# Kernel tuning notes

Measured on AMD Instinct MI355X. Metric: run time of the kernel, lower is better.

Reference implementation:

```python
import jax, jax.numpy as jnp
import numpy as np

N_NODES = 50000


def _segment_mean(vals, seg_ids, num_segments):
    s = jax.ops.segment_sum(vals, seg_ids, num_segments=num_segments)
    cnt = jax.ops.segment_sum(jnp.ones((vals.shape[0],), vals.dtype), seg_ids,
                              num_segments=num_segments)
    return s / jnp.clip(cnt, 1.0)[:, None]


def _sage_layer(h, src, dst, W_self, W_neigh, b):
    # mean-aggregate neighbor messages: gather h[src], scatter-mean to dst
    neigh = _segment_mean(h[src], dst, N_NODES)
    return h @ W_self + neigh @ W_neigh + b


def _edge_score(h, src, dst, Wp, bp):
    # concat(h_u, h_v) @ Wp == h_u @ Wp[:d] + h_v @ Wp[d:]
    d = h.shape[1]
    return h[src] @ Wp[:d] + h[dst] @ Wp[d:] + bp


def setup_inputs() -> dict:
    key = jax.random.key(0)
    ks = jax.random.split(key, 16)
    N, E, EP, EN = N_NODES, 800000, 200000, 200000
    d_in, d_hid, d_out = 128, 256, 128
    inp = {
        'x': jax.random.normal(ks[0], (N, d_in), jnp.float32),
        'msg_src': jax.random.randint(ks[1], (E,), 0, N, jnp.int32),
        'msg_dst': jax.random.randint(ks[2], (E,), 0, N, jnp.int32),
        'pos_src': jax.random.randint(ks[3], (EP,), 0, N, jnp.int32),
        'pos_dst': jax.random.randint(ks[4], (EP,), 0, N, jnp.int32),
        'neg_src': jax.random.randint(ks[5], (EN,), 0, N, jnp.int32),
        'neg_dst': jax.random.randint(ks[6], (EN,), 0, N, jnp.int32),
        'W1_self': jax.random.normal(ks[7], (d_in, d_hid), jnp.float32) * 0.05,
        'W1_neigh': jax.random.normal(ks[8], (d_in, d_hid), jnp.float32) * 0.05,
        'b1': jnp.zeros((d_hid,), jnp.float32),
        'W2_self': jax.random.normal(ks[9], (d_hid, d_out), jnp.float32) * 0.05,
        'W2_neigh': jax.random.normal(ks[10], (d_hid, d_out), jnp.float32) * 0.05,
        'b2': jnp.zeros((d_out,), jnp.float32),
        'Wp': jax.random.normal(ks[11], (2 * d_out, 1), jnp.float32) * 0.05,
        'bp': jnp.zeros((1,), jnp.float32),
    }
    return inp


def reference(x, msg_src, msg_dst, pos_src, pos_dst, neg_src, neg_dst,
              W1_self, W1_neigh, b1, W2_self, W2_neigh, b2, Wp, bp):
    h = _sage_layer(x, msg_src, msg_dst, W1_self, W1_neigh, b1)
    h = jax.nn.relu(h)
    h = _sage_layer(h, msg_src, msg_dst, W2_self, W2_neigh, b2)
    pos_score = _edge_score(h, pos_src, pos_dst, Wp, bp)
    neg_score = _edge_score(h, neg_src, neg_dst, Wp, bp)
    return pos_score, neg_score
```

## Files before the change

### kernel.cpp

```cpp
#include <hip/hip_runtime.h>


#define NN 50000
#define EM 800000
#define EPOS 200000
#define ENEG 200000
#define NB 196
#define RPB 4096
#define MTILES 3125
#define GEMM_GRID 512

typedef __bf16 bf16;
typedef bf16 bf16x2 __attribute__((ext_vector_type(2)));
typedef bf16 bf16x4 __attribute__((ext_vector_type(4)));
typedef bf16 bf16x8 __attribute__((ext_vector_type(8)));
typedef float floatx4 __attribute__((ext_vector_type(4)));

#define I_CNT  0
#define I_ROW  50176
#define I_BSUM 100608
#define I_BOFF 100864
#define I_CCUR 101120
#define I_CSR  101376
#define B_CREG 3605504
#define B_XB   10005504
#define B_AGG1 22805504
#define B_H1   35605504
#define B_NV   61205504
#define B_WT1  62005504
#define B_WT2  62136576
#define B_P    62267648
#define B_Q    62468352

__global__ __launch_bounds__(256) void count_kernel(const int* __restrict__ dst,
                                                    int* __restrict__ cnt, int n) {
    int i = blockIdx.x * blockDim.x + threadIdx.x;
    if (i < n) atomicAdd(&cnt[dst[i]], 1);
}

__global__ __launch_bounds__(256) void scan1_kernel(const int* __restrict__ cnt,
                                                    int* __restrict__ bsum) {
    __shared__ int s[256];
    int t = threadIdx.x;
    int i = blockIdx.x * 256 + t;
    s[t] = (i < NN) ? cnt[i] : 0;
    __syncthreads();
    for (int o = 128; o > 0; o >>= 1) {
        if (t < o) s[t] += s[t + o];
        __syncthreads();
    }
    if (t == 0) bsum[blockIdx.x] = s[0];
}

__global__ __launch_bounds__(256) void scan2_kernel(const int* __restrict__ bsum,
                                                    int* __restrict__ boff) {
    __shared__ int s[256];
    int t = threadIdx.x;
    s[t] = (t < NB) ? bsum[t] : 0;
    __syncthreads();
    for (int o = 1; o < 256; o <<= 1) {
        int u = (t >= o) ? s[t - o] : 0;
        __syncthreads();
        s[t] += u;
        __syncthreads();
    }
    if (t < NB) boff[t] = (t == 0) ? 0 : s[t - 1];
}

__global__ __launch_bounds__(256) void scan3_kernel(const int* __restrict__ cnt,
                                                    const int* __restrict__ boff,
                                                    int* __restrict__ rowstart,
                                                    int* __restrict__ ccur) {
    __shared__ int s[256];
    int t = threadIdx.x;
    int i = blockIdx.x * 256 + t;
    int v = (i < NN) ? cnt[i] : 0;
    s[t] = v;
    __syncthreads();
    for (int o = 1; o < 256; o <<= 1) {
        int u = (t >= o) ? s[t - o] : 0;
        __syncthreads();
        s[t] += u;
        __syncthreads();
    }
    int excl = boff[blockIdx.x] + s[t] - v;
    if (i < NN) rowstart[i] = excl;
    if (i == NN - 1) rowstart[NN] = EM;
    if (t == 0) ccur[blockIdx.x] = boff[blockIdx.x];
}

__global__ __launch_bounds__(256) void bin_kernel(const int* __restrict__ src,
                                                  const int* __restrict__ dst,
                                                  int* __restrict__ ccur,
                                                  unsigned long long* __restrict__ creg) {
    __shared__ int hist[NB];
    __shared__ int cnt2[NB];
    __shared__ int goff[NB];
    __shared__ int base[256];
    __shared__ unsigned long long sorted[RPB];
    int t = threadIdx.x;
    int e0 = blockIdx.x * RPB;
    int nrec = EM - e0; if (nrec > RPB) nrec = RPB;

    for (int i = t; i < NB; i += 256) { hist[i] = 0; cnt2[i] = 0; }
    __syncthreads();

    int myb[RPB / 256];
    unsigned long long myrec[RPB / 256];
#pragma unroll
    for (int j = 0; j < RPB / 256; ++j) {
        int idx = j * 256 + t;
        if (idx < nrec) {
            int s = src[e0 + idx], d = dst[e0 + idx];
            myb[j] = d >> 8;
            myrec[j] = ((unsigned long long)(unsigned)d << 32) | (unsigned)s;
            atomicAdd(&hist[myb[j]], 1);
        } else myb[j] = -1;
    }
    __syncthreads();

    base[t] = (t < NB) ? hist[t] : 0;
    __syncthreads();
    for (int o = 1; o < 256; o <<= 1) {
        int u = (t >= o) ? base[t - o] : 0;
        __syncthreads();
        base[t] += u;
        __syncthreads();
    }

    if (t < NB && hist[t] > 0) goff[t] = atomicAdd(&ccur[t], hist[t]);
#pragma unroll
    for (int j = 0; j < RPB / 256; ++j) {
        if (myb[j] >= 0) {
            int rk = atomicAdd(&cnt2[myb[j]], 1);
            sorted[base[myb[j]] - hist[myb[j]] + rk] = myrec[j];
        }
    }
    __syncthreads();

#pragma unroll
    for (int j = 0; j < RPB / 256; ++j) {
        int idx = j * 256 + t;
        if (idx < nrec) {
            unsigned long long rec = sorted[idx];
            int b = (int)(rec >> 40);
            int exb = base[b] - hist[b];
            creg[(size_t)goff[b] + (idx - exb)] = rec;
        }
    }
}

__global__ __launch_bounds__(256) void binsort_kernel(
    const unsigned long long* __restrict__ creg,
    const int* __restrict__ rowstart, int* __restrict__ csr) {
    __shared__ int lcur[256];
    int t = threadIdx.x;
    int node0 = blockIdx.x * 256;
    int nodes = NN - node0; if (nodes > 256) nodes = 256;
    if (t < nodes) lcur[t] = rowstart[node0 + t];
    __syncthreads();
    int beg = rowstart[node0];
    int end = rowstart[node0 + nodes];
    for (int i = beg + t; i < end; i += 256) {
        unsigned long long rec = creg[i];
        int s = (int)(rec & 0xffffffffu);
        int d = (int)(rec >> 32);
        int pos = atomicAdd(&lcur[d - node0], 1);
        csr[pos] = s;
    }
}

__global__ __launch_bounds__(256) void convx_kernel(const float* __restrict__ x,
                                                    bf16* __restrict__ xb) {
    int i = blockIdx.x * 256 + threadIdx.x;
    if (i >= NN * 128 / 4) return;
    float4 v = ((const float4*)x)[i];
    bf16x4 o;
    o[0] = (bf16)v.x; o[1] = (bf16)v.y; o[2] = (bf16)v.z; o[3] = (bf16)v.w;
    *(bf16x4*)(xb + (size_t)i * 4) = o;
}

__global__ __launch_bounds__(256) void convw_kernel(
    const float* __restrict__ W1s, const float* __restrict__ W1n,
    const float* __restrict__ W2n, const float* __restrict__ W2s,
    bf16* __restrict__ Wt1, bf16* __restrict__ Wt2) {
    int i = blockIdx.x * 256 + threadIdx.x;
    if (i >= 65536) return;
    int n = i >> 8, k = i & 255;
    float w1 = (k < 128) ? W1s[k * 256 + n] : W1n[(k - 128) * 256 + n];
    Wt1[i] = (bf16)w1;
    float w2 = (n < 128) ? W2n[k * 128 + n] : W2s[k * 128 + (n - 128)];
    Wt2[i] = (bf16)w2;
}

__global__ __launch_bounds__(256) void gather1_kernel(const bf16* __restrict__ feat,
                                                      const int* __restrict__ rowstart,
                                                      const int* __restrict__ csr,
                                                      bf16* __restrict__ agg) {
    int node = (blockIdx.x * 256 + threadIdx.x) >> 6;
    if (node >= NN) return;
    int lane = threadIdx.x & 63;
    int c = lane * 2;
    int beg = rowstart[node], end = rowstart[node + 1];
    float ax = 0.f, ay = 0.f;
    int i = beg;
    for (; i + 7 < end; i += 8) {
        float lx = 0.f, ly = 0.f;
#pragma unroll
        for (int u = 0; u < 8; ++u) {
            int s = csr[i + u];
            bf16x2 v = *(const bf16x2*)(feat + (size_t)s * 128 + c);
            lx += (float)v[0];
            ly += (float)v[1];
        }
        ax += lx; ay += ly;
    }
    for (; i < end; ++i) {
        int s = csr[i];
        bf16x2 v = *(const bf16x2*)(feat + (size_t)s * 128 + c);
        ax += (float)v[0];
        ay += (float)v[1];
    }
    int deg = end - beg;
    float inv = 1.0f / (float)(deg > 0 ? deg : 1);
    bf16x2 o;
    o[0] = (bf16)(ax * inv);
    o[1] = (bf16)(ay * inv);
    *(bf16x2*)(agg + (size_t)node * 128 + c) = o;
}

__global__ __launch_bounds__(256) void gemm1_kernel(
    const bf16* __restrict__ xb, const bf16* __restrict__ aggb,
    const bf16* __restrict__ Wt, const float* __restrict__ b1,
    bf16* __restrict__ h1b) {
    int w = threadIdx.x >> 6;
    int lane = threadIdx.x & 63;
    int r = lane & 15, quad = lane >> 4;
    int colbase = w * 64;

    bf16x8 bfr[4][8];
#pragma unroll
    for (int t = 0; t < 4; ++t)
#pragma unroll
        for (int kk = 0; kk < 8; ++kk)
            bfr[t][kk] = *(const bf16x8*)(Wt + (size_t)(colbase + t * 16 + r) * 256
                                          + kk * 32 + quad * 8);
    float bb[4];
#pragma unroll
    for (int t = 0; t < 4; ++t) bb[t] = b1[colbase + t * 16 + r];

    for (int tile = blockIdx.x; tile < MTILES; tile += GEMM_GRID) {
        int m0 = tile * 16;
        int row = m0 + r;
        bf16x8 a[8];
#pragma unroll
        for (int kk = 0; kk < 4; ++kk)
            a[kk] = *(const bf16x8*)(xb + (size_t)row * 128 + kk * 32 + quad * 8);
#pragma unroll
        for (int kk = 4; kk < 8; ++kk)
            a[kk] = *(const bf16x8*)(aggb + (size_t)row * 128 + (kk - 4) * 32 + quad * 8);
        floatx4 acc[4];
#pragma unroll
        for (int t = 0; t < 4; ++t) acc[t] = (floatx4){0.f, 0.f, 0.f, 0.f};
#pragma unroll
        for (int kk = 0; kk < 8; ++kk)
#pragma unroll
            for (int t = 0; t < 4; ++t)
                acc[t] = __builtin_amdgcn_mfma_f32_16x16x32_bf16(a[kk], bfr[t][kk],
                                                                 acc[t], 0, 0, 0);
        int mb = m0 + quad * 4;
#pragma unroll
        for (int t = 0; t < 4; ++t) {
            int col = colbase + t * 16 + r;
#pragma unroll
            for (int rr = 0; rr < 4; ++rr) {
                float v = acc[t][rr] + bb[t];
                v = v > 0.f ? v : 0.f;
                h1b[(size_t)(mb + rr) * 256 + col] = (bf16)v;
            }
        }
    }
}

__global__ __launch_bounds__(256) void gemm2_kernel(
    const bf16* __restrict__ h1b, const bf16* __restrict__ Wt,
    const float* __restrict__ b2, const float* __restrict__ wp,
    float4* __restrict__ nodev) {
    __shared__ float lp[4][16];
    __shared__ float lq[4][16];
    int w = threadIdx.x >> 6;
    int lane = threadIdx.x & 63;
    int r = lane & 15, quad = lane >> 4;
    int colbase = w * 64;

    bf16x8 bfr[4][8];
#pragma unroll
    for (int t = 0; t < 4; ++t)
#pragma unroll
        for (int kk = 0; kk < 8; ++kk)
            bfr[t][kk] = *(const bf16x8*)(Wt + (size_t)(colbase + t * 16 + r) * 256
                                          + kk * 32 + quad * 8);
    float bb[4], wA[4], wB[4];
#pragma unroll
    for (int t = 0; t < 4; ++t) {
        int col = colbase + t * 16 + r;
        if (w < 2) {
            bb[t] = 0.f;
            wA[t] = wp[col];
            wB[t] = wp[128 + col];
        } else {
            int c2 = col - 128;
            bb[t] = b2[c2];
            wA[t] = wp[c2];
            wB[t] = wp[128 + c2];
        }
    }

    for (int tile = blockIdx.x; tile < MTILES; tile += GEMM_GRID) {
        int m0 = tile * 16;
        int row = m0 + r;
        bf16x8 a[8];
#pragma unroll
        for (int kk = 0; kk < 8; ++kk)
            a[kk] = *(const bf16x8*)(h1b + (size_t)row * 256 + kk * 32 + quad * 8);
        floatx4 acc[4];
#pragma unroll
        for (int t = 0; t < 4; ++t) acc[t] = (floatx4){0.f, 0.f, 0.f, 0.f};
#pragma unroll
        for (int kk = 0; kk < 8; ++kk)
#pragma unroll
            for (int t = 0; t < 4; ++t)
                acc[t] = __builtin_amdgcn_mfma_f32_16x16x32_bf16(a[kk], bfr[t][kk],
                                                                 acc[t], 0, 0, 0);
        float pacc[4], qacc[4];
#pragma unroll
        for (int rr = 0; rr < 4; ++rr) {
            float pr = 0.f, qr = 0.f;
#pragma unroll
            for (int t = 0; t < 4; ++t) {
                float v = acc[t][rr] + bb[t];
                pr += v * wA[t];
                qr += v * wB[t];
            }
            pacc[rr] = pr;
            qacc[rr] = qr;
        }
#pragma unroll
        for (int m = 1; m <= 8; m <<= 1) {
#pragma unroll
            for (int rr = 0; rr < 4; ++rr) {
                pacc[rr] += __shfl_xor(pacc[rr], m);
                qacc[rr] += __shfl_xor(qacc[rr], m);
            }
        }
        if (r == 0) {
#pragma unroll
            for (int rr = 0; rr < 4; ++rr) {
                lp[w][quad * 4 + rr] = pacc[rr];
                lq[w][quad * 4 + rr] = qacc[rr];
            }
        }
        __syncthreads();
        if (threadIdx.x < 16) {
            int rw = threadIdx.x;
            float4 o;
            o.x = lp[0][rw] + lp[1][rw];
            o.y = lq[0][rw] + lq[1][rw];
            o.z = lp[2][rw] + lp[3][rw];
            o.w = lq[2][rw] + lq[3][rw];
            nodev[m0 + rw] = o;
        }
        __syncthreads();
    }
}

__global__ __launch_bounds__(256) void gather2_kernel(
    const float4* __restrict__ nodev, const int* __restrict__ rowstart,
    const int* __restrict__ csr, float* __restrict__ p, float* __restrict__ q) {
    int t = threadIdx.x;
    int node = blockIdx.x * 16 + (t >> 4);
    if (node >= NN) return;
    int l = t & 15;
    int beg = rowstart[node], end = rowstart[node + 1];
    float pz = 0.f, qz = 0.f;
    for (int i = beg + l; i < end; i += 16) {
        float4 v = nodev[csr[i]];
        pz += v.x;
        qz += v.y;
    }
#pragma unroll
    for (int m = 8; m >= 1; m >>= 1) {
        pz += __shfl_xor(pz, m);
        qz += __shfl_xor(qz, m);
    }
    if (l == 0) {
        int deg = end - beg;
        float inv = 1.0f / (float)(deg > 0 ? deg : 1);
        float4 me = nodev[node];
        p[node] = me.z + pz * inv;
        q[node] = me.w + qz * inv;
    }
}

__global__ __launch_bounds__(256) void score_kernel(
    const int* __restrict__ psrc, const int* __restrict__ pdst,
    const int* __restrict__ nsrc, const int* __restrict__ ndst,
    const float* __restrict__ p, const float* __restrict__ q,
    const float* __restrict__ bp, float* __restrict__ out) {
    int i = blockIdx.x * blockDim.x + threadIdx.x;
    float b = bp[0];
    if (i < EPOS) {
        out[i] = p[psrc[i]] + q[pdst[i]] + b;
    } else if (i < EPOS + ENEG) {
        int j = i - EPOS;
        out[i] = p[nsrc[j]] + q[ndst[j]] + b;
    }
}

extern "C" void kernel_launch(void* const* d_in, const int* in_sizes, int n_in,
                              void* d_out, int out_size, void* d_ws, size_t ws_size,
                              hipStream_t stream) {
    const float* x    = (const float*)d_in[0];
    const int*   msrc = (const int*)d_in[1];
    const int*   mdst = (const int*)d_in[2];
    const int*   psrc = (const int*)d_in[3];
    const int*   pdst = (const int*)d_in[4];
    const int*   nsrc = (const int*)d_in[5];
    const int*   ndst = (const int*)d_in[6];
    const float* W1s  = (const float*)d_in[7];
    const float* W1n  = (const float*)d_in[8];
    const float* b1   = (const float*)d_in[9];
    const float* W2s  = (const float*)d_in[10];
    const float* W2n  = (const float*)d_in[11];
    const float* b2   = (const float*)d_in[12];
    const float* wp   = (const float*)d_in[13];
    const float* bp   = (const float*)d_in[14];

    char* ws = (char*)d_ws;
    int*   cnt      = (int*)ws + I_CNT;
    int*   rowstart = (int*)ws + I_ROW;
    int*   bsum     = (int*)ws + I_BSUM;
    int*   boff     = (int*)ws + I_BOFF;
    int*   ccur     = (int*)ws + I_CCUR;
    int*   csr_src  = (int*)ws + I_CSR;
    unsigned long long* creg = (unsigned long long*)(ws + B_CREG);
    bf16*   xb    = (bf16*)(ws + B_XB);
    bf16*   agg1b = (bf16*)(ws + B_AGG1);
    bf16*   h1b   = (bf16*)(ws + B_H1);
    float4* nodev = (float4*)(ws + B_NV);
    bf16*   Wt1   = (bf16*)(ws + B_WT1);
    bf16*   Wt2   = (bf16*)(ws + B_WT2);
    float*  p     = (float*)(ws + B_P);
    float*  q     = (float*)(ws + B_Q);
    float*  out   = (float*)d_out;

    hipMemsetAsync(cnt, 0, 50176 * sizeof(int), stream);

    count_kernel<<<(EM + 255) / 256, 256, 0, stream>>>(mdst, cnt, EM);
    scan1_kernel<<<NB, 256, 0, stream>>>(cnt, bsum);
    scan2_kernel<<<1, 256, 0, stream>>>(bsum, boff);
    scan3_kernel<<<NB, 256, 0, stream>>>(cnt, boff, rowstart, ccur);
    bin_kernel<<<(EM + RPB - 1) / RPB, 256, 0, stream>>>(msrc, mdst, ccur, creg);
    binsort_kernel<<<NB, 256, 0, stream>>>(creg, rowstart, csr_src);

    convx_kernel<<<6250, 256, 0, stream>>>(x, xb);
    convw_kernel<<<256, 256, 0, stream>>>(W1s, W1n, W2n, W2s, Wt1, Wt2);

    gather1_kernel<<<(NN * 64 + 255) / 256, 256, 0, stream>>>(xb, rowstart, csr_src, agg1b);
    gemm1_kernel<<<GEMM_GRID, 256, 0, stream>>>(xb, agg1b, Wt1, b1, h1b);
    gemm2_kernel<<<GEMM_GRID, 256, 0, stream>>>(h1b, Wt2, b2, wp, nodev);
    gather2_kernel<<<(NN + 15) / 16, 256, 0, stream>>>(nodev, rowstart, csr_src, p, q);
    score_kernel<<<(EPOS + ENEG + 255) / 256, 256, 0, stream>>>(
        psrc, pdst, nsrc, ndst, p, q, bp, out);
}
```

Measured before the change: 267.9 us.

## Store x and layer-1 aggregate in column-blocked layout for cache-local gathers

The bf16 copy of x and the layer-1 aggregate now use a column-blocked layout: 8 slices of 16 columns, each holding all nodes contiguously. The layer-1 gather runs one column slice per block, so the working set each block touches (50000×32 bytes) can stay in cache. Each node's edges are spread over 16 lane pairs that load 16-byte vectors and then reduce with shuffles. The x and weight conversion kernels are merged into one launch, and the GEMM A-operand loads are adapted to the new layout. The risks are redundant rowstart/csr reads across the 8 slices and less coalesced A loads in gemm1.

```diff
diff --git a/kernel.cpp b/kernel.cpp
--- a/kernel.cpp
+++ b/kernel.cpp
@@ -9,6 +9,7 @@
 #define RPB 4096
 #define MTILES 3125
 #define GEMM_GRID 512
+#define XCONV_BLOCKS 6250
 
 typedef __bf16 bf16;
 typedef bf16 bf16x2 __attribute__((ext_vector_type(2)));
@@ -23,8 +24,8 @@
 #define I_CCUR 101120
 #define I_CSR  101376
 #define B_CREG 3605504
-#define B_XB   10005504
-#define B_AGG1 22805504
+#define B_XCB  10005504
+#define B_ACB  22805504
 #define B_H1   35605504
 #define B_NV   61205504
 #define B_WT1  62005504
@@ -170,67 +171,73 @@
     }
 }
 
-__global__ __launch_bounds__(256) void convx_kernel(const float* __restrict__ x,
-                                                    bf16* __restrict__ xb) {
-    int i = blockIdx.x * 256 + threadIdx.x;
-    if (i >= NN * 128 / 4) return;
-    float4 v = ((const float4*)x)[i];
-    bf16x4 o;
-    o[0] = (bf16)v.x; o[1] = (bf16)v.y; o[2] = (bf16)v.z; o[3] = (bf16)v.w;
-    *(bf16x4*)(xb + (size_t)i * 4) = o;
-}
-
-__global__ __launch_bounds__(256) void convw_kernel(
+__global__ __launch_bounds__(256) void conv_kernel(
+    const float* __restrict__ x, bf16* __restrict__ xcb,
     const float* __restrict__ W1s, const float* __restrict__ W1n,
     const float* __restrict__ W2n, const float* __restrict__ W2s,
     bf16* __restrict__ Wt1, bf16* __restrict__ Wt2) {
-    int i = blockIdx.x * 256 + threadIdx.x;
-    if (i >= 65536) return;
-    int n = i >> 8, k = i & 255;
-    float w1 = (k < 128) ? W1s[k * 256 + n] : W1n[(k - 128) * 256 + n];
-    Wt1[i] = (bf16)w1;
-    float w2 = (n < 128) ? W2n[k * 128 + n] : W2s[k * 128 + (n - 128)];
-    Wt2[i] = (bf16)w2;
-}
-
-__global__ __launch_bounds__(256) void gather1_kernel(const bf16* __restrict__ feat,
+    if (blockIdx.x < XCONV_BLOCKS) {
+        int i = blockIdx.x * 256 + threadIdx.x;
+        float4 v = ((const float4*)x)[i];
+        int e = i * 4;
+        int n = e >> 7, c = e & 127;
+        bf16x4 o;
+        o[0] = (bf16)v.x; o[1] = (bf16)v.y; o[2] = (bf16)v.z; o[3] = (bf16)v.w;
+        *(bf16x4*)(xcb + ((size_t)(c >> 4) * NN + n) * 16 + (c & 15)) = o;
+    } else {
+        int i = (blockIdx.x - XCONV_BLOCKS) * 256 + threadIdx.x;
+        if (i >= 65536) return;
+        int n = i >> 8, k = i & 255;
+        float w1 = (k < 128) ? W1s[k * 256 + n] : W1n[(k - 128) * 256 + n];
+        Wt1[i] = (bf16)w1;
+        float w2 = (n < 128) ? W2n[k * 128 + n] : W2s[k * 128 + (n - 128)];
+        Wt2[i] = (bf16)w2;
+    }
+}
+
+__global__ __launch_bounds__(256) void gather1_kernel(const bf16* __restrict__ xcb,
                                                       const int* __restrict__ rowstart,
                                                       const int* __restrict__ csr,
-                                                      bf16* __restrict__ agg) {
-    int node = (blockIdx.x * 256 + threadIdx.x) >> 6;
-    if (node >= NN) return;
+                                                      bf16* __restrict__ aggcb) {
+    int cblk = blockIdx.x & 7;
+    int chunk = blockIdx.x >> 3;
     int lane = threadIdx.x & 63;
-    int c = lane * 2;
-    int beg = rowstart[node], end = rowstart[node + 1];
-    float ax = 0.f, ay = 0.f;
-    int i = beg;
-    for (; i + 7 < end; i += 8) {
-        float lx = 0.f, ly = 0.f;
-#pragma unroll
-        for (int u = 0; u < 8; ++u) {
-            int s = csr[i + u];
-            bf16x2 v = *(const bf16x2*)(feat + (size_t)s * 128 + c);
-            lx += (float)v[0];
-            ly += (float)v[1];
-        }
-        ax += lx; ay += ly;
-    }
-    for (; i < end; ++i) {
-        int s = csr[i];
-        bf16x2 v = *(const bf16x2*)(feat + (size_t)s * 128 + c);
-        ax += (float)v[0];
-        ay += (float)v[1];
-    }
-    int deg = end - beg;
-    float inv = 1.0f / (float)(deg > 0 ? deg : 1);
-    bf16x2 o;
-    o[0] = (bf16)(ax * inv);
-    o[1] = (bf16)(ay * inv);
-    *(bf16x2*)(agg + (size_t)node * 128 + c) = o;
+    int wave = threadIdx.x >> 6;
+    int half = lane >> 5;
+    int hl = lane & 31;
+    int l2 = hl >> 1, h = hl & 1;
+    const bf16* slice = xcb + (size_t)cblk * NN * 16;
+    bf16* oslice = aggcb + (size_t)cblk * NN * 16;
+    int nodebase = chunk * 64 + wave * 16 + half * 8;
+#pragma unroll
+    for (int j = 0; j < 8; ++j) {
+        int n = nodebase + j;
+        if (n >= NN) return;
+        int beg = rowstart[n], end = rowstart[n + 1];
+        float acc[8] = {0.f, 0.f, 0.f, 0.f, 0.f, 0.f, 0.f, 0.f};
+        for (int i = beg + l2; i < end; i += 16) {
+            int s = csr[i];
+            bf16x8 v = *(const bf16x8*)(slice + (size_t)s * 16 + h * 8);
+#pragma unroll
+            for (int u = 0; u < 8; ++u) acc[u] += (float)v[u];
+        }
+#pragma unroll
+        for (int m = 2; m <= 16; m <<= 1)
+#pragma unroll
+            for (int u = 0; u < 8; ++u) acc[u] += __shfl_xor(acc[u], m);
+        if (l2 == 0) {
+            int deg = end - beg;
+            float inv = 1.0f / (float)(deg > 0 ? deg : 1);
+            bf16x8 o;
+#pragma unroll
+            for (int u = 0; u < 8; ++u) o[u] = (bf16)(acc[u] * inv);
+            *(bf16x8*)(oslice + (size_t)n * 16 + h * 8) = o;
+        }
+    }
 }
 
 __global__ __launch_bounds__(256) void gemm1_kernel(
-    const bf16* __restrict__ xb, const bf16* __restrict__ aggb,
+    const bf16* __restrict__ xcb, const bf16* __restrict__ aggcb,
     const bf16* __restrict__ Wt, const float* __restrict__ b1,
     bf16* __restrict__ h1b) {
     int w = threadIdx.x >> 6;
@@ -249,16 +256,18 @@
 #pragma unroll
     for (int t = 0; t < 4; ++t) bb[t] = b1[colbase + t * 16 + r];
 
+    int blk = quad >> 1;
+    int off = (quad & 1) * 8;
     for (int tile = blockIdx.x; tile < MTILES; tile += GEMM_GRID) {
         int m0 = tile * 16;
         int row = m0 + r;
         bf16x8 a[8];
 #pragma unroll
         for (int kk = 0; kk < 4; ++kk)
-            a[kk] = *(const bf16x8*)(xb + (size_t)row * 128 + kk * 32 + quad * 8);
+            a[kk] = *(const bf16x8*)(xcb + ((size_t)(kk * 2 + blk) * NN + row) * 16 + off);
 #pragma unroll
         for (int kk = 4; kk < 8; ++kk)
-            a[kk] = *(const bf16x8*)(aggb + (size_t)row * 128 + (kk - 4) * 32 + quad * 8);
+            a[kk] = *(const bf16x8*)(aggcb + ((size_t)((kk - 4) * 2 + blk) * NN + row) * 16 + off);
         floatx4 acc[4];
 #pragma unroll
         for (int t = 0; t < 4; ++t) acc[t] = (floatx4){0.f, 0.f, 0.f, 0.f};
@@ -444,8 +453,8 @@
     int*   ccur     = (int*)ws + I_CCUR;
     int*   csr_src  = (int*)ws + I_CSR;
     unsigned long long* creg = (unsigned long long*)(ws + B_CREG);
-    bf16*   xb    = (bf16*)(ws + B_XB);
-    bf16*   agg1b = (bf16*)(ws + B_AGG1);
+    bf16*   xcb   = (bf16*)(ws + B_XCB);
+    bf16*   aggcb = (bf16*)(ws + B_ACB);
     bf16*   h1b   = (bf16*)(ws + B_H1);
     float4* nodev = (float4*)(ws + B_NV);
     bf16*   Wt1   = (bf16*)(ws + B_WT1);
@@ -463,11 +472,12 @@
     bin_kernel<<<(EM + RPB - 1) / RPB, 256, 0, stream>>>(msrc, mdst, ccur, creg);
     binsort_kernel<<<NB, 256, 0, stream>>>(creg, rowstart, csr_src);
 
-    convx_kernel<<<6250, 256, 0, stream>>>(x, xb);
-    convw_kernel<<<256, 256, 0, stream>>>(W1s, W1n, W2n, W2s, Wt1, Wt2);
-
-    gather1_kernel<<<(NN * 64 + 255) / 256, 256, 0, stream>>>(xb, rowstart, csr_src, agg1b);
-    gemm1_kernel<<<GEMM_GRID, 256, 0, stream>>>(xb, agg1b, Wt1, b1, h1b);
+    conv_kernel<<<XCONV_BLOCKS + 256, 256, 0, stream>>>(x, xcb, W1s, W1n, W2n, W2s,
+                                                        Wt1, Wt2);
+
+    gather1_kernel<<<((NN + 63) / 64) * 8, 256, 0, stream>>>(xcb, rowstart, csr_src,
+                                                             aggcb);
+    gemm1_kernel<<<GEMM_GRID, 256, 0, stream>>>(xcb, aggcb, Wt1, b1, h1b);
     gemm2_kernel<<<GEMM_GRID, 256, 0, stream>>>(h1b, Wt2, b2, wp, nodev);
     gather2_kernel<<<(NN + 15) / 16, 256, 0, stream>>>(nodev, rowstart, csr_src, p, q);
     score_kernel<<<(EPOS + ENEG + 255) / 256, 256, 0, stream>>>(
```

After: 302.1 us. 1.13x slower.
